# Kernel tuning notes

Hardware: AMD Instinct MI355X
Metric: run time of the kernel (lower is better)

Reference implementation:

```python
import jax, jax.numpy as jnp
import numpy as np

H_SP, W_SP = 8, 8
NUM_HEADS = 6
SHARED = 96
DIM_Q, DIM_KV = 96, 192
WIN = H_SP * W_SP  # 64 tokens per window


def _rel_index():
    # Swin-style relative position index, static numpy computation
    coords = np.stack(np.meshgrid(np.arange(H_SP), np.arange(W_SP), indexing='ij'))
    cf = coords.reshape(2, -1)                      # [2, 64]
    rel = cf[:, :, None] - cf[:, None, :]           # [2, 64, 64]
    rel = rel.transpose(1, 2, 0).astype(np.int64)   # [64, 64, 2]
    rel[..., 0] += H_SP - 1
    rel[..., 1] += W_SP - 1
    rel[..., 0] *= 2 * W_SP - 1
    return rel.sum(-1)                              # [64, 64], values in [0, 225)

REL_IDX = jnp.asarray(_rel_index())


def setup_inputs() -> dict:
    key = jax.random.key(0)
    ks = jax.random.split(key, 12)
    B, H, W = 4, 256, 256
    f32 = jnp.float32
    std = 0.02
    return {
        'x_q':  jax.random.normal(ks[0], (B, DIM_Q, H, W), f32),
        'x_kv': jax.random.normal(ks[1], (B, DIM_KV, H, W), f32),
        'Wq': jax.random.normal(ks[2], (DIM_Q, SHARED), f32) * std,
        'bq': jnp.zeros((SHARED,), f32),
        'Wk': jax.random.normal(ks[3], (DIM_KV, SHARED), f32) * std,
        'bk': jnp.zeros((SHARED,), f32),
        'Wv': jax.random.normal(ks[4], (DIM_KV, SHARED), f32) * std,
        'bv': jnp.zeros((SHARED,), f32),
        'bias_table': jax.random.normal(ks[5], ((2 * H_SP - 1) * (2 * W_SP - 1), NUM_HEADS), f32) * std,
        'Wo': jax.random.normal(ks[6], (SHARED, DIM_Q), f32) * std,
        'bo': jnp.zeros((DIM_Q,), f32),
    }


def reference(x_q, x_kv, Wq, bq, Wk, bk, Wv, bv, bias_table, Wo, bo):
    B, Cq, H, W = x_q.shape
    nH, nW = H // H_SP, W // W_SP  # H, W divisible by window -> pad is a no-op
    hd = SHARED // NUM_HEADS
    scale = hd ** -0.5

    def to_windows(img):
        C = img.shape[1]
        x = img.reshape(B, C, nH, H_SP, nW, W_SP)
        return x.transpose(0, 2, 4, 3, 5, 1).reshape(-1, WIN, C)

    qw = to_windows(x_q)    # [nWin, 64, Cq]
    kvw = to_windows(x_kv)  # [nWin, 64, Ckv]

    def heads(x):
        return x.reshape(-1, WIN, NUM_HEADS, hd).transpose(0, 2, 1, 3)  # [nWin, h, 64, hd]

    q = heads(qw @ Wq + bq)
    k = heads(kvw @ Wk + bk)
    v = heads(kvw @ Wv + bv)

    attn = jnp.einsum('whqd,whkd->whqk', q, k) * scale  # [nWin, h, 64, 64]
    rel_bias = bias_table[REL_IDX].transpose(2, 0, 1)   # [h, 64, 64]
    attn = jax.nn.softmax(attn + rel_bias[None], axis=-1)

    out = jnp.einsum('whqk,whkd->whqd', attn, v)        # [nWin, h, 64, hd]
    out = out.transpose(0, 2, 1, 3).reshape(-1, WIN, SHARED)
    out = out @ Wo + bo                                 # [nWin, 64, Cq]

    # windows2img
    out = out.reshape(B, nH, nW, H_SP, W_SP, Cq)
    out = out.transpose(0, 1, 3, 2, 4, 5).reshape(B, H, W, Cq)
    return out.transpose(0, 3, 1, 2)  # [B, Cq, H, W]
```

## Files before the change

kernel.cpp:

```cpp
#include <hip/hip_runtime.h>

typedef short short8 __attribute__((ext_vector_type(8)));
typedef float f32x4 __attribute__((ext_vector_type(4)));
typedef unsigned short ushort;

#define MFMA(a, b, c) __builtin_amdgcn_mfma_f32_16x16x32_bf16(a, b, c, 0, 0, 0)

#define WS_WQT 0
#define WS_WKT 9216
#define WS_WVT 27648
#define WS_WOT 46080
#define WS_BIAS 55296
#define WS_TOTAL 56646

#define STR_A 104
#define OFF_A 0
#define OFF_K16 13312
#define OFF_VT 25600
#define STR_VT 72
#define OFF_PQ 39424
#define P_STRIDE 72
#define OFF_BIAS 50688
#define LDS_BYTES 53392

__device__ __forceinline__ ushort f2bf(float x) {
    unsigned u = __float_as_uint(x);
    u = (u + 0x7FFFu + ((u >> 16) & 1u)) >> 16;
    return (ushort)u;
}
__device__ __forceinline__ float bf2f(ushort u) {
    return __uint_as_float(((unsigned)u) << 16);
}

__global__ void prep_weights(const float* __restrict__ Wq, const float* __restrict__ Wk,
                             const float* __restrict__ Wv, const float* __restrict__ Wo,
                             const float* __restrict__ btab, ushort* __restrict__ ws) {
    int idx = blockIdx.x * 256 + threadIdx.x;
    if (idx < WS_WKT) {
        int f = idx >> 9, w = idx & 511, lane = w >> 3, j = w & 7;
        int nt = f / 3, kt = f % 3;
        int n = nt * 16 + (lane & 15), k = kt * 32 + (lane >> 4) * 8 + j;
        ws[idx] = f2bf(Wq[k * 96 + n]);
    } else if (idx < WS_WVT) {
        int t = idx - WS_WKT;
        int f = t >> 9, w = t & 511, lane = w >> 3, j = w & 7;
        int kt6 = f / 6, nt = f % 6;
        int n = nt * 16 + (lane & 15), k = kt6 * 32 + (lane >> 4) * 8 + j;
        ws[idx] = f2bf(Wk[k * 96 + n]);
    } else if (idx < WS_WOT) {
        int t = idx - WS_WVT;
        int f = t >> 9, w = t & 511, lane = w >> 3, j = w & 7;
        int kt6 = f / 6, nt = f % 6;
        int n = nt * 16 + (lane & 15), k = kt6 * 32 + (lane >> 4) * 8 + j;
        ws[idx] = f2bf(Wv[k * 96 + n]);
    } else if (idx < WS_BIAS) {
        int t = idx - WS_WOT;
        int f = t >> 9, w = t & 511, lane = w >> 3, j = w & 7;
        int nt = f / 3, kt = f % 3;
        int n = nt * 16 + (lane & 15), k = kt * 32 + (lane >> 4) * 8 + j;
        ws[idx] = f2bf(Wo[k * 96 + n]);
    } else if (idx < WS_TOTAL) {
        ws[idx] = f2bf(btab[idx - WS_BIAS]);
    }
}

__global__ __launch_bounds__(256, 3) void swin_attn(
    const float* __restrict__ xq, const float* __restrict__ xkv,
    const float* __restrict__ bq, const float* __restrict__ bk,
    const float* __restrict__ bv, const float* __restrict__ bo,
    const ushort* __restrict__ ws, float* __restrict__ out)
{
    __shared__ __align__(16) char smem[LDS_BYTES];
    const int tid = threadIdx.x;
    const int wave = tid >> 6, lane = tid & 63;
    const int l15 = lane & 15, quad = lane >> 4;
    int wid = ((blockIdx.x & 7) << 9) | (blockIdx.x >> 3);
    const int b = wid >> 10;
    const int wh = (wid >> 5) & 31, ww = wid & 31;
    const int h0 = wh * 8, w0 = ww * 8;
    const int mt = wave;

    ushort* A     = (ushort*)(smem + OFF_A);
    ushort* k16   = (ushort*)(smem + OFF_K16);
    ushort* vt    = (ushort*)(smem + OFF_VT);
    ushort* ps    = (ushort*)(smem + OFF_PQ) + wave * (16 * P_STRIDE);
    ushort* qsc   = (ushort*)(smem + OFF_PQ + 9216) + wave * 256;
    ushort* biasl = (ushort*)(smem + OFF_BIAS);

    float bqr[6], bkr[6], bvr[6], bor[6];
    #pragma unroll
    for (int h = 0; h < 6; ++h) {
        bqr[h] = bq[h * 16 + l15]; bkr[h] = bk[h * 16 + l15];
        bvr[h] = bv[h * 16 + l15]; bor[h] = bo[h * 16 + l15];
    }

    int pc[3], pi[3];
    #pragma unroll
    for (int t = 0; t < 3; ++t) { int p = tid + t * 256; pc[t] = p % 96; pi[t] = p / 96; }

    const float* xkvb = xkv + (size_t)b * 192 * 65536;
    float4 pf[3][2];
    #pragma unroll
    for (int t = 0; t < 3; ++t) {
        const float* g = xkvb + (size_t)pc[t] * 65536 + (h0 + pi[t]) * 256 + w0;
        pf[t][0] = *(const float4*)g; pf[t][1] = *(const float4*)(g + 4);
    }
    for (int i = tid; i < 1350; i += 256) biasl[i] = ws[WS_BIAS + i];

    #pragma unroll
    for (int t = 0; t < 3; ++t) {
        int base = (pi[t] * 8) * STR_A + pc[t];
        A[base]             = f2bf(pf[t][0].x); A[base + STR_A]     = f2bf(pf[t][0].y);
        A[base + 2 * STR_A] = f2bf(pf[t][0].z); A[base + 3 * STR_A] = f2bf(pf[t][0].w);
        A[base + 4 * STR_A] = f2bf(pf[t][1].x); A[base + 5 * STR_A] = f2bf(pf[t][1].y);
        A[base + 6 * STR_A] = f2bf(pf[t][1].z); A[base + 7 * STR_A] = f2bf(pf[t][1].w);
    }
    __syncthreads();

    float4 pg[3][2];
    #pragma unroll
    for (int t = 0; t < 3; ++t) {
        const float* g = xkvb + (size_t)(96 + pc[t]) * 65536 + (h0 + pi[t]) * 256 + w0;
        pg[t][0] = *(const float4*)g; pg[t][1] = *(const float4*)(g + 4);
    }

    f32x4 accK[6], accV[6];
    #pragma unroll
    for (int n = 0; n < 6; ++n) { accK[n] = {}; accV[n] = {}; }
    const int arow = (mt * 16 + l15) * STR_A + quad * 8;
    #pragma unroll
    for (int kt = 0; kt < 3; ++kt) {
        short8 a = *(const short8*)(A + arow + kt * 32);
        #pragma unroll
        for (int nt = 0; nt < 6; ++nt) {
            short8 bk8 = *(const short8*)(ws + WS_WKT + (((kt * 6) + nt) * 64 + lane) * 8);
            accK[nt] = MFMA(a, bk8, accK[nt]);
            short8 bv8 = *(const short8*)(ws + WS_WVT + (((kt * 6) + nt) * 64 + lane) * 8);
            accV[nt] = MFMA(a, bv8, accV[nt]);
        }
    }
    __syncthreads();

    #pragma unroll
    for (int t = 0; t < 3; ++t) {
        int base = (pi[t] * 8) * STR_A + pc[t];
        A[base]             = f2bf(pg[t][0].x); A[base + STR_A]     = f2bf(pg[t][0].y);
        A[base + 2 * STR_A] = f2bf(pg[t][0].z); A[base + 3 * STR_A] = f2bf(pg[t][0].w);
        A[base + 4 * STR_A] = f2bf(pg[t][1].x); A[base + 5 * STR_A] = f2bf(pg[t][1].y);
        A[base + 6 * STR_A] = f2bf(pg[t][1].z); A[base + 7 * STR_A] = f2bf(pg[t][1].w);
    }
    __syncthreads();

    const float* xqb = xq + (size_t)b * 96 * 65536;
    #pragma unroll
    for (int t = 0; t < 3; ++t) {
        const float* g = xqb + (size_t)pc[t] * 65536 + (h0 + pi[t]) * 256 + w0;
        pf[t][0] = *(const float4*)g; pf[t][1] = *(const float4*)(g + 4);
    }

    #pragma unroll
    for (int kt = 0; kt < 3; ++kt) {
        short8 a = *(const short8*)(A + arow + kt * 32);
        #pragma unroll
        for (int nt = 0; nt < 6; ++nt) {
            short8 bk8 = *(const short8*)(ws + WS_WKT + ((((3 + kt) * 6) + nt) * 64 + lane) * 8);
            accK[nt] = MFMA(a, bk8, accK[nt]);
            short8 bv8 = *(const short8*)(ws + WS_WVT + ((((3 + kt) * 6) + nt) * 64 + lane) * 8);
            accV[nt] = MFMA(a, bv8, accV[nt]);
        }
    }
    #pragma unroll
    for (int nt = 0; nt < 6; ++nt) {
        ushort* dk = k16 + nt * (64 * 16) + (mt * 16 + quad * 4) * 16 + l15;
        ushort* dv = vt + nt * (16 * STR_VT) + l15 * STR_VT + (mt * 16 + quad * 4);
        #pragma unroll
        for (int r = 0; r < 4; ++r) {
            dk[r * 16] = f2bf(accK[nt][r] + bkr[nt]);
            dv[r]      = f2bf(accV[nt][r] + bvr[nt]);
        }
    }
    __syncthreads();

    #pragma unroll
    for (int t = 0; t < 3; ++t) {
        int base = (pi[t] * 8) * STR_A + pc[t];
        A[base]             = f2bf(pf[t][0].x); A[base + STR_A]     = f2bf(pf[t][0].y);
        A[base + 2 * STR_A] = f2bf(pf[t][0].z); A[base + 3 * STR_A] = f2bf(pf[t][0].w);
        A[base + 4 * STR_A] = f2bf(pf[t][1].x); A[base + 5 * STR_A] = f2bf(pf[t][1].y);
        A[base + 6 * STR_A] = f2bf(pf[t][1].z); A[base + 7 * STR_A] = f2bf(pf[t][1].w);
    }
    __syncthreads();

    const int qtok0 = mt * 16 + quad * 4;
    int bidx[4][4];
    #pragma unroll
    for (int nt = 0; nt < 4; ++nt) {
        int kt2 = nt * 16 + l15, i2 = kt2 >> 3, j2 = kt2 & 7;
        #pragma unroll
        for (int r = 0; r < 4; ++r) {
            int qt = qtok0 + r, i1 = qt >> 3, j1 = qt & 7;
            bidx[nt][r] = ((i1 - i2 + 7) * 15 + (j1 - j2 + 7)) * 6;
        }
    }

    f32x4 accO[6];
    short8 zero8 = {};
    for (int h = 0; h < 6; ++h) {
        f32x4 qa = {};
        #pragma unroll
        for (int kt = 0; kt < 3; ++kt) {
            short8 a  = *(const short8*)(A + arow + kt * 32);
            short8 bb = *(const short8*)(ws + WS_WQT + ((h * 3 + kt) * 64 + lane) * 8);
            qa = MFMA(a, bb, qa);
        }
        #pragma unroll
        for (int r = 0; r < 4; ++r)
            qsc[(quad * 4 + r) * 16 + l15] = f2bf((qa[r] + bqr[h]) * 0.25f);

        short8 aq = zero8;
        if (quad < 2) aq = *(const short8*)(qsc + l15 * 16 + quad * 8);
        f32x4 s[4];
        #pragma unroll
        for (int nt = 0; nt < 4; ++nt) {
            short8 bk8 = zero8;
            if (quad < 2) bk8 = *(const short8*)(k16 + h * (64 * 16) + (nt * 16 + l15) * 16 + quad * 8);
            f32x4 z = {};
            s[nt] = MFMA(aq, bk8, z);
        }
        #pragma unroll
        for (int nt = 0; nt < 4; ++nt)
            #pragma unroll
            for (int r = 0; r < 4; ++r)
                s[nt][r] += bf2f(biasl[bidx[nt][r] + h]);
        float pr[4][4];
        #pragma unroll
        for (int r = 0; r < 4; ++r) {
            float m = fmaxf(fmaxf(s[0][r], s[1][r]), fmaxf(s[2][r], s[3][r]));
            m = fmaxf(m, __shfl_xor(m, 1)); m = fmaxf(m, __shfl_xor(m, 2));
            m = fmaxf(m, __shfl_xor(m, 4)); m = fmaxf(m, __shfl_xor(m, 8));
            float l = 0.f;
            #pragma unroll
            for (int nt = 0; nt < 4; ++nt) { pr[nt][r] = __expf(s[nt][r] - m); l += pr[nt][r]; }
            l += __shfl_xor(l, 1); l += __shfl_xor(l, 2);
            l += __shfl_xor(l, 4); l += __shfl_xor(l, 8);
            float inv = 1.0f / l;
            #pragma unroll
            for (int nt = 0; nt < 4; ++nt) pr[nt][r] *= inv;
        }
        #pragma unroll
        for (int nt = 0; nt < 4; ++nt)
            #pragma unroll
            for (int r = 0; r < 4; ++r)
                ps[(quad * 4 + r) * P_STRIDE + nt * 16 + l15] = f2bf(pr[nt][r]);
        f32x4 o = {};
        #pragma unroll
        for (int k2 = 0; k2 < 2; ++k2) {
            short8 ap  = *(const short8*)(ps + l15 * P_STRIDE + k2 * 32 + quad * 8);
            short8 bv8 = *(const short8*)(vt + h * (16 * STR_VT) + l15 * STR_VT + k2 * 32 + quad * 8);
            o = MFMA(ap, bv8, o);
        }
        accO[h] = o;
    }
    __syncthreads();

    ushort* obuf = A;
    #pragma unroll
    for (int h = 0; h < 6; ++h)
        #pragma unroll
        for (int r = 0; r < 4; ++r)
            obuf[(mt * 16 + quad * 4 + r) * STR_A + h * 16 + l15] = f2bf(accO[h][r]);

    {
        int t0 = mt * 16 + quad * 4;
        int i = t0 >> 3, j0 = t0 & 7;
        #pragma unroll
        for (int nt = 0; nt < 6; ++nt) {
            f32x4 acc = {};
            #pragma unroll
            for (int kt = 0; kt < 3; ++kt) {
                short8 a  = *(const short8*)(obuf + arow + kt * 32);
                short8 bb = *(const short8*)(ws + WS_WOT + ((nt * 3 + kt) * 64 + lane) * 8);
                acc = MFMA(a, bb, acc);
            }
            int cout = nt * 16 + l15;
            float4 v4 = make_float4(acc[0] + bor[nt], acc[1] + bor[nt], acc[2] + bor[nt], acc[3] + bor[nt]);
            float* dst = out + (size_t)(b * 96 + cout) * 65536 + (h0 + i) * 256 + w0 + j0;
            *(float4*)dst = v4;
        }
    }
}

extern "C" void kernel_launch(void* const* d_in, const int* in_sizes, int n_in,
                              void* d_out, int out_size, void* d_ws, size_t ws_size,
                              hipStream_t stream) {
    const float* xq   = (const float*)d_in[0];
    const float* xkv  = (const float*)d_in[1];
    const float* Wq   = (const float*)d_in[2];
    const float* bq   = (const float*)d_in[3];
    const float* Wk   = (const float*)d_in[4];
    const float* bk   = (const float*)d_in[5];
    const float* Wv   = (const float*)d_in[6];
    const float* bv   = (const float*)d_in[7];
    const float* btab = (const float*)d_in[8];
    const float* Wo   = (const float*)d_in[9];
    const float* bo   = (const float*)d_in[10];
    ushort* ws = (ushort*)d_ws;
    float* out = (float*)d_out;

    hipLaunchKernelGGL(prep_weights, dim3((WS_TOTAL + 255) / 256), dim3(256), 0, stream,
                       Wq, Wk, Wv, Wo, btab, ws);
    hipLaunchKernelGGL(swin_attn, dim3(4096), dim3(256), 0, stream,
                       xq, xkv, bq, bk, bv, bo, ws, out);
}
```

Measured before the change: 513.6 us.

## Split fused window attention into projection, attention and output-projection kernels

```diff
diff --git a/kernel.cpp b/kernel.cpp
--- a/kernel.cpp
+++ b/kernel.cpp
@@ -6,65 +6,326 @@
 
 #define MFMA(a, b, c) __builtin_amdgcn_mfma_f32_16x16x32_bf16(a, b, c, 0, 0, 0)
 
-#define WS_WQT 0
-#define WS_WKT 9216
-#define WS_WVT 27648
-#define WS_WOT 46080
-#define WS_BIAS 55296
-#define WS_TOTAL 56646
-
+__device__ __forceinline__ ushort f2bf(float x) {
+    unsigned u = __float_as_uint(x);
+    u = (u + 0x7FFFu + ((u >> 16) & 1u)) >> 16;
+    return (ushort)u;
+}
+__device__ __forceinline__ float bf2f(ushort u) {
+    return __uint_as_float(((unsigned)u) << 16);
+}
+
+#define WS_Q   0
+#define WS_KV  9216
+#define WS_O   46080
+#define WS_BT  55296
+#define WS_BIG 56648
+#define QBUF_OFF  WS_BIG
+#define KVBUF_OFF (WS_BIG + 25165824)
+#define ABUF_OFF  (KVBUF_OFF + 50331648)
+#define NEED_BYTES ((size_t)(ABUF_OFF + 25165824) * 2)
+
+__global__ void prep_w(const float* __restrict__ Wq, const float* __restrict__ Wk,
+                       const float* __restrict__ Wv, const float* __restrict__ Wo,
+                       const float* __restrict__ btab, ushort* __restrict__ ws) {
+    int idx = blockIdx.x * 256 + threadIdx.x;
+    if (idx < WS_KV) {
+        int f = idx >> 9, w = idx & 511, lane = w >> 3, j = w & 7;
+        int kt = f / 6, nt = f % 6;
+        int cout = nt * 16 + (lane & 15), c = kt * 32 + (lane >> 4) * 8 + j;
+        ws[idx] = f2bf(Wq[c * 96 + cout] * 0.25f);
+    } else if (idx < WS_O) {
+        int t = idx - WS_KV; int f = t >> 9, w = t & 511, lane = w >> 3, j = w & 7;
+        int kt6 = f / 12, nt = f % 12;
+        int cout = nt * 16 + (lane & 15), c = kt6 * 32 + (lane >> 4) * 8 + j;
+        float v = (cout < 96) ? Wk[c * 96 + cout] : Wv[c * 96 + (cout - 96)];
+        ws[idx] = f2bf(v);
+    } else if (idx < WS_BT) {
+        int t = idx - WS_O; int f = t >> 9, w = t & 511, lane = w >> 3, j = w & 7;
+        int kt = f / 6, mt = f % 6;
+        int m = mt * 16 + (lane & 15), k = kt * 32 + (lane >> 4) * 8 + j;
+        ws[idx] = f2bf(Wo[k * 96 + m]);
+    } else if (idx < WS_BIG) {
+        if (idx < WS_BT + 1350) ws[idx] = f2bf(btab[idx - WS_BT]);
+    }
+}
+
+__global__ __launch_bounds__(256, 4) void k2_proj(
+    const float* __restrict__ xq, const float* __restrict__ xkv,
+    const float* __restrict__ bq, const float* __restrict__ bk,
+    const float* __restrict__ bv, const ushort* __restrict__ ws,
+    ushort* __restrict__ qbuf, ushort* __restrict__ kvbuf)
+{
+    __shared__ ushort At[64 * 104];
+    const int tid = threadIdx.x;
+    const int wave = tid >> 6, lane = tid & 63, l15 = lane & 15, quad = lane >> 4;
+    const bool isQ = blockIdx.x < 4096;
+    const int g = isQ ? blockIdx.x : blockIdx.x - 4096;
+    const int b = g >> 10, tok0 = (g & 1023) * 64;
+    const int arow = (wave * 16 + l15) * 104 + quad * 8;
+    const int trow = tok0 + wave * 16 + quad * 4;
+
+    if (isQ) {
+        const float* src = xq + (size_t)b * 96 * 65536;
+        #pragma unroll 4
+        for (int p = 0; p < 24; ++p) {
+            int c = p * 4 + wave;
+            At[lane * 104 + c] = f2bf(src[c * 65536 + tok0 + lane]);
+        }
+        __syncthreads();
+        f32x4 acc[6];
+        #pragma unroll
+        for (int n = 0; n < 6; ++n) acc[n] = {};
+        #pragma unroll
+        for (int kt = 0; kt < 3; ++kt) {
+            short8 a = *(const short8*)(At + arow + kt * 32);
+            #pragma unroll
+            for (int nt = 0; nt < 6; ++nt) {
+                short8 w8 = *(const short8*)(ws + WS_Q + ((kt * 6 + nt) * 64 + lane) * 8);
+                acc[nt] = MFMA(a, w8, acc[nt]);
+            }
+        }
+        ushort* dst = qbuf + ((size_t)b * 65536 + trow) * 96;
+        #pragma unroll
+        for (int nt = 0; nt < 6; ++nt) {
+            float bias = bq[nt * 16 + l15] * 0.25f;
+            #pragma unroll
+            for (int r = 0; r < 4; ++r)
+                dst[r * 96 + nt * 16 + l15] = f2bf(acc[nt][r] + bias);
+        }
+    } else {
+        const float* src = xkv + (size_t)b * 192 * 65536;
+        f32x4 acc[12];
+        #pragma unroll
+        for (int n = 0; n < 12; ++n) acc[n] = {};
+        for (int half = 0; half < 2; ++half) {
+            if (half) __syncthreads();
+            const float* s2 = src + half * 96 * 65536;
+            #pragma unroll 4
+            for (int p = 0; p < 24; ++p) {
+                int c = p * 4 + wave;
+                At[lane * 104 + c] = f2bf(s2[c * 65536 + tok0 + lane]);
+            }
+            __syncthreads();
+            #pragma unroll
+            for (int kt = 0; kt < 3; ++kt) {
+                short8 a = *(const short8*)(At + arow + kt * 32);
+                int kt6 = half * 3 + kt;
+                #pragma unroll
+                for (int nt = 0; nt < 12; ++nt) {
+                    short8 w8 = *(const short8*)(ws + WS_KV + ((kt6 * 12 + nt) * 64 + lane) * 8);
+                    acc[nt] = MFMA(a, w8, acc[nt]);
+                }
+            }
+        }
+        ushort* dst = kvbuf + ((size_t)b * 65536 + trow) * 192;
+        #pragma unroll
+        for (int nt = 0; nt < 12; ++nt) {
+            int cout = nt * 16 + l15;
+            float bias = (cout < 96) ? bk[cout] : bv[cout - 96];
+            #pragma unroll
+            for (int r = 0; r < 4; ++r)
+                dst[r * 192 + cout] = f2bf(acc[nt][r] + bias);
+        }
+    }
+}
+
+#define K3_VT 0
+#define K3_PS 13824
+#define K3_BIAS 26112
+#define K3_LDS 28812
+
+__global__ __launch_bounds__(256, 4) void k3_attn(
+    const ushort* __restrict__ ws, const ushort* __restrict__ qbuf,
+    const ushort* __restrict__ kvbuf, ushort* __restrict__ abuf)
+{
+    __shared__ __align__(16) char smem[K3_LDS];
+    ushort* vt    = (ushort*)smem;
+    ushort* biasl = (ushort*)(smem + K3_BIAS);
+    const int tid = threadIdx.x;
+    const int wave = tid >> 6, lane = tid & 63, l15 = lane & 15, quad = lane >> 4;
+    const int wid = blockIdx.x;
+    const int b = wid >> 10, wh = (wid >> 5) & 31, ww = wid & 31;
+    const int wb = b * 65536 + (wh * 8) * 256 + ww * 8;
+
+    for (int i = tid; i < 1350; i += 256) biasl[i] = ws[WS_BT + i];
+    {
+        int tok = tid >> 2, cc = tid & 3;
+        int tg = wb + (tok >> 3) * 256 + (tok & 7);
+        const ushort* vrow = kvbuf + (size_t)tg * 192 + 96;
+        #pragma unroll
+        for (int rd = 0; rd < 3; ++rd) {
+            int vd0 = (rd * 4 + cc) * 8;
+            short8 v8 = *(const short8*)(vrow + vd0);
+            #pragma unroll
+            for (int e = 0; e < 8; ++e)
+                vt[(vd0 + e) * 72 + tok] = (ushort)v8[e];
+        }
+    }
+    const int myq = wave * 16 + l15;
+    const size_t qrow = ((size_t)(wb + (myq >> 3) * 256 + (myq & 7))) * 96;
+    size_t krow[4];
+    #pragma unroll
+    for (int nt = 0; nt < 4; ++nt) {
+        int kt2 = nt * 16 + l15;
+        krow[nt] = ((size_t)(wb + (kt2 >> 3) * 256 + (kt2 & 7))) * 192;
+    }
+    const int qtok0 = wave * 16 + quad * 4;
+    int bidx[4][4];
+    #pragma unroll
+    for (int nt = 0; nt < 4; ++nt) {
+        int kt2 = nt * 16 + l15, i2 = kt2 >> 3, j2 = kt2 & 7;
+        #pragma unroll
+        for (int r = 0; r < 4; ++r) {
+            int qt = qtok0 + r, i1 = qt >> 3, j1 = qt & 7;
+            bidx[nt][r] = ((i1 - i2 + 7) * 15 + (j1 - j2 + 7)) * 6;
+        }
+    }
+    __syncthreads();
+
+    ushort* ps = (ushort*)(smem + K3_PS) + wave * 1152;
+    f32x4 accO[6];
+    short8 zero8 = {};
+    for (int h = 0; h < 6; ++h) {
+        short8 aq = zero8;
+        if (quad < 2) aq = *(const short8*)(qbuf + qrow + h * 16 + quad * 8);
+        f32x4 s[4];
+        #pragma unroll
+        for (int nt = 0; nt < 4; ++nt) {
+            short8 bk8 = zero8;
+            if (quad < 2) bk8 = *(const short8*)(kvbuf + krow[nt] + h * 16 + quad * 8);
+            f32x4 z = {};
+            s[nt] = MFMA(aq, bk8, z);
+        }
+        #pragma unroll
+        for (int nt = 0; nt < 4; ++nt)
+            #pragma unroll
+            for (int r = 0; r < 4; ++r)
+                s[nt][r] += bf2f(biasl[bidx[nt][r] + h]);
+        float pr[4][4];
+        #pragma unroll
+        for (int r = 0; r < 4; ++r) {
+            float m = fmaxf(fmaxf(s[0][r], s[1][r]), fmaxf(s[2][r], s[3][r]));
+            m = fmaxf(m, __shfl_xor(m, 1)); m = fmaxf(m, __shfl_xor(m, 2));
+            m = fmaxf(m, __shfl_xor(m, 4)); m = fmaxf(m, __shfl_xor(m, 8));
+            float l = 0.f;
+            #pragma unroll
+            for (int nt = 0; nt < 4; ++nt) { pr[nt][r] = __expf(s[nt][r] - m); l += pr[nt][r]; }
+            l += __shfl_xor(l, 1); l += __shfl_xor(l, 2);
+            l += __shfl_xor(l, 4); l += __shfl_xor(l, 8);
+            float inv = 1.0f / l;
+            #pragma unroll
+            for (int nt = 0; nt < 4; ++nt) pr[nt][r] *= inv;
+        }
+        #pragma unroll
+        for (int nt = 0; nt < 4; ++nt)
+            #pragma unroll
+            for (int r = 0; r < 4; ++r)
+                ps[(quad * 4 + r) * 72 + nt * 16 + l15] = f2bf(pr[nt][r]);
+        f32x4 o = {};
+        #pragma unroll
+        for (int k2 = 0; k2 < 2; ++k2) {
+            short8 ap  = *(const short8*)(ps + l15 * 72 + k2 * 32 + quad * 8);
+            short8 bv8 = *(const short8*)(vt + (h * 16 + l15) * 72 + k2 * 32 + quad * 8);
+            o = MFMA(ap, bv8, o);
+        }
+        accO[h] = o;
+    }
+    __syncthreads();
+
+    ushort* obuf = (ushort*)(smem + K3_PS);
+    #pragma unroll
+    for (int h = 0; h < 6; ++h)
+        #pragma unroll
+        for (int r = 0; r < 4; ++r)
+            obuf[(wave * 16 + quad * 4 + r) * 96 + h * 16 + l15] = f2bf(accO[h][r]);
+    #pragma unroll
+    for (int e = 0; e < 3; ++e) {
+        int cid = e * 64 + lane;
+        int tr = wave * 16 + cid / 12, c8 = cid % 12;
+        short8 o8 = *(const short8*)(obuf + tr * 96 + c8 * 8);
+        int tg = wb + (tr >> 3) * 256 + (tr & 7);
+        *(short8*)(abuf + (size_t)tg * 96 + c8 * 8) = o8;
+    }
+}
+
+__global__ __launch_bounds__(256, 4) void k4_out(
+    const ushort* __restrict__ ws, const ushort* __restrict__ abuf,
+    const float* __restrict__ bo, float* __restrict__ out)
+{
+    const int tid = threadIdx.x;
+    const int wave = tid >> 6, lane = tid & 63, l15 = lane & 15, quad = lane >> 4;
+    const int wtok = blockIdx.x * 64 + wave * 16;
+    const ushort* arow = abuf + (size_t)(wtok + l15) * 96;
+    f32x4 acc[6];
+    #pragma unroll
+    for (int m = 0; m < 6; ++m) acc[m] = {};
+    #pragma unroll
+    for (int kt = 0; kt < 3; ++kt) {
+        short8 bfrag = *(const short8*)(arow + kt * 32 + quad * 8);
+        #pragma unroll
+        for (int mt = 0; mt < 6; ++mt) {
+            short8 a8 = *(const short8*)(ws + WS_O + ((kt * 6 + mt) * 64 + lane) * 8);
+            acc[mt] = MFMA(a8, bfrag, acc[mt]);
+        }
+    }
+    const int b = wtok >> 16, rem = wtok & 65535;
+    #pragma unroll
+    for (int mt = 0; mt < 6; ++mt) {
+        float4 bo4 = *(const float4*)(bo + mt * 16 + quad * 4);
+        float bv[4] = {bo4.x, bo4.y, bo4.z, bo4.w};
+        #pragma unroll
+        for (int r = 0; r < 4; ++r) {
+            int cout = mt * 16 + quad * 4 + r;
+            out[(size_t)(b * 96 + cout) * 65536 + rem + l15] = acc[mt][r] + bv[r];
+        }
+    }
+}
+
+#define FB_WQT 0
+#define FB_WKT 9216
+#define FB_WVT 27648
+#define FB_WOT 46080
+#define FB_BIAS 55296
+#define FB_TOTAL 56646
 #define STR_A 104
 #define OFF_A 0
 #define OFF_K16 13312
 #define OFF_VT 25600
-#define STR_VT 72
 #define OFF_PQ 39424
-#define P_STRIDE 72
 #define OFF_BIAS 50688
 #define LDS_BYTES 53392
 
-__device__ __forceinline__ ushort f2bf(float x) {
-    unsigned u = __float_as_uint(x);
-    u = (u + 0x7FFFu + ((u >> 16) & 1u)) >> 16;
-    return (ushort)u;
-}
-__device__ __forceinline__ float bf2f(ushort u) {
-    return __uint_as_float(((unsigned)u) << 16);
-}
-
-__global__ void prep_weights(const float* __restrict__ Wq, const float* __restrict__ Wk,
-                             const float* __restrict__ Wv, const float* __restrict__ Wo,
-                             const float* __restrict__ btab, ushort* __restrict__ ws) {
+__global__ void prep_w_fb(const float* __restrict__ Wq, const float* __restrict__ Wk,
+                          const float* __restrict__ Wv, const float* __restrict__ Wo,
+                          const float* __restrict__ btab, ushort* __restrict__ ws) {
     int idx = blockIdx.x * 256 + threadIdx.x;
-    if (idx < WS_WKT) {
+    if (idx < FB_WKT) {
         int f = idx >> 9, w = idx & 511, lane = w >> 3, j = w & 7;
         int nt = f / 3, kt = f % 3;
         int n = nt * 16 + (lane & 15), k = kt * 32 + (lane >> 4) * 8 + j;
         ws[idx] = f2bf(Wq[k * 96 + n]);
-    } else if (idx < WS_WVT) {
-        int t = idx - WS_WKT;
-        int f = t >> 9, w = t & 511, lane = w >> 3, j = w & 7;
+    } else if (idx < FB_WVT) {
+        int t = idx - FB_WKT; int f = t >> 9, w = t & 511, lane = w >> 3, j = w & 7;
         int kt6 = f / 6, nt = f % 6;
         int n = nt * 16 + (lane & 15), k = kt6 * 32 + (lane >> 4) * 8 + j;
         ws[idx] = f2bf(Wk[k * 96 + n]);
-    } else if (idx < WS_WOT) {
-        int t = idx - WS_WVT;
-        int f = t >> 9, w = t & 511, lane = w >> 3, j = w & 7;
+    } else if (idx < FB_WOT) {
+        int t = idx - FB_WVT; int f = t >> 9, w = t & 511, lane = w >> 3, j = w & 7;
         int kt6 = f / 6, nt = f % 6;
         int n = nt * 16 + (lane & 15), k = kt6 * 32 + (lane >> 4) * 8 + j;
         ws[idx] = f2bf(Wv[k * 96 + n]);
-    } else if (idx < WS_BIAS) {
-        int t = idx - WS_WOT;
-        int f = t >> 9, w = t & 511, lane = w >> 3, j = w & 7;
+    } else if (idx < FB_BIAS) {
+        int t = idx - FB_WOT; int f = t >> 9, w = t & 511, lane = w >> 3, j = w & 7;
         int nt = f / 3, kt = f % 3;
         int n = nt * 16 + (lane & 15), k = kt * 32 + (lane >> 4) * 8 + j;
         ws[idx] = f2bf(Wo[k * 96 + n]);
-    } else if (idx < WS_TOTAL) {
-        ws[idx] = f2bf(btab[idx - WS_BIAS]);
-    }
-}
-
-__global__ __launch_bounds__(256, 3) void swin_attn(
+    } else if (idx < FB_TOTAL) {
+        ws[idx] = f2bf(btab[idx - FB_BIAS]);
+    }
+}
+
+__global__ __launch_bounds__(256, 3) void swin_attn_fb(
     const float* __restrict__ xq, const float* __restrict__ xkv,
     const float* __restrict__ bq, const float* __restrict__ bk,
     const float* __restrict__ bv, const float* __restrict__ bo,
@@ -79,25 +340,21 @@
     const int wh = (wid >> 5) & 31, ww = wid & 31;
     const int h0 = wh * 8, w0 = ww * 8;
     const int mt = wave;
-
     ushort* A     = (ushort*)(smem + OFF_A);
     ushort* k16   = (ushort*)(smem + OFF_K16);
     ushort* vt    = (ushort*)(smem + OFF_VT);
-    ushort* ps    = (ushort*)(smem + OFF_PQ) + wave * (16 * P_STRIDE);
+    ushort* ps    = (ushort*)(smem + OFF_PQ) + wave * (16 * 72);
     ushort* qsc   = (ushort*)(smem + OFF_PQ + 9216) + wave * 256;
     ushort* biasl = (ushort*)(smem + OFF_BIAS);
-
     float bqr[6], bkr[6], bvr[6], bor[6];
     #pragma unroll
     for (int h = 0; h < 6; ++h) {
         bqr[h] = bq[h * 16 + l15]; bkr[h] = bk[h * 16 + l15];
         bvr[h] = bv[h * 16 + l15]; bor[h] = bo[h * 16 + l15];
     }
-
     int pc[3], pi[3];
     #pragma unroll
     for (int t = 0; t < 3; ++t) { int p = tid + t * 256; pc[t] = p % 96; pi[t] = p / 96; }
-
     const float* xkvb = xkv + (size_t)b * 192 * 65536;
     float4 pf[3][2];
     #pragma unroll
@@ -105,25 +362,22 @@
         const float* g = xkvb + (size_t)pc[t] * 65536 + (h0 + pi[t]) * 256 + w0;
         pf[t][0] = *(const float4*)g; pf[t][1] = *(const float4*)(g + 4);
     }
-    for (int i = tid; i < 1350; i += 256) biasl[i] = ws[WS_BIAS + i];
-
+    for (int i = tid; i < 1350; i += 256) biasl[i] = ws[FB_BIAS + i];
     #pragma unroll
     for (int t = 0; t < 3; ++t) {
         int base = (pi[t] * 8) * STR_A + pc[t];
-        A[base]             = f2bf(pf[t][0].x); A[base + STR_A]     = f2bf(pf[t][0].y);
+        A[base] = f2bf(pf[t][0].x); A[base + STR_A] = f2bf(pf[t][0].y);
         A[base + 2 * STR_A] = f2bf(pf[t][0].z); A[base + 3 * STR_A] = f2bf(pf[t][0].w);
         A[base + 4 * STR_A] = f2bf(pf[t][1].x); A[base + 5 * STR_A] = f2bf(pf[t][1].y);
         A[base + 6 * STR_A] = f2bf(pf[t][1].z); A[base + 7 * STR_A] = f2bf(pf[t][1].w);
     }
     __syncthreads();
-
     float4 pg[3][2];
     #pragma unroll
     for (int t = 0; t < 3; ++t) {
         const float* g = xkvb + (size_t)(96 + pc[t]) * 65536 + (h0 + pi[t]) * 256 + w0;
         pg[t][0] = *(const float4*)g; pg[t][1] = *(const float4*)(g + 4);
     }
-
     f32x4 accK[6], accV[6];
     #pragma unroll
     for (int n = 0; n < 6; ++n) { accK[n] = {}; accV[n] = {}; }
@@ -133,46 +387,43 @@
         short8 a = *(const short8*)(A + arow + kt * 32);
         #pragma unroll
         for (int nt = 0; nt < 6; ++nt) {
-            short8 bk8 = *(const short8*)(ws + WS_WKT + (((kt * 6) + nt) * 64 + lane) * 8);
+            short8 bk8 = *(const short8*)(ws + FB_WKT + (((kt * 6) + nt) * 64 + lane) * 8);
             accK[nt] = MFMA(a, bk8, accK[nt]);
-            short8 bv8 = *(const short8*)(ws + WS_WVT + (((kt * 6) + nt) * 64 + lane) * 8);
+            short8 bv8 = *(const short8*)(ws + FB_WVT + (((kt * 6) + nt) * 64 + lane) * 8);
             accV[nt] = MFMA(a, bv8, accV[nt]);
         }
     }
     __syncthreads();
-
     #pragma unroll
     for (int t = 0; t < 3; ++t) {
         int base = (pi[t] * 8) * STR_A + pc[t];
-        A[base]             = f2bf(pg[t][0].x); A[base + STR_A]     = f2bf(pg[t][0].y);
+        A[base] = f2bf(pg[t][0].x); A[base + STR_A] = f2bf(pg[t][0].y);
         A[base + 2 * STR_A] = f2bf(pg[t][0].z); A[base + 3 * STR_A] = f2bf(pg[t][0].w);
         A[base + 4 * STR_A] = f2bf(pg[t][1].x); A[base + 5 * STR_A] = f2bf(pg[t][1].y);
         A[base + 6 * STR_A] = f2bf(pg[t][1].z); A[base + 7 * STR_A] = f2bf(pg[t][1].w);
     }
     __syncthreads();
-
     const float* xqb = xq + (size_t)b * 96 * 65536;
     #pragma unroll
     for (int t = 0; t < 3; ++t) {
         const float* g = xqb + (size_t)pc[t] * 65536 + (h0 + pi[t]) * 256 + w0;
         pf[t][0] = *(const float4*)g; pf[t][1] = *(const float4*)(g + 4);
     }
-
     #pragma unroll
     for (int kt = 0; kt < 3; ++kt) {
         short8 a = *(const short8*)(A + arow + kt * 32);
         #pragma unroll
         for (int nt = 0; nt < 6; ++nt) {
-            short8 bk8 = *(const short8*)(ws + WS_WKT + ((((3 + kt) * 6) + nt) * 64 + lane) * 8);
+            short8 bk8 = *(const short8*)(ws + FB_WKT + ((((3 + kt) * 6) + nt) * 64 + lane) * 8);
             accK[nt] = MFMA(a, bk8, accK[nt]);
-            short8 bv8 = *(const short8*)(ws + WS_WVT + ((((3 + kt) * 6) + nt) * 64 + lane) * 8);
+            short8 bv8 = *(const short8*)(ws + FB_WVT + ((((3 + kt) * 6) + nt) * 64 + lane) * 8);
             accV[nt] = MFMA(a, bv8, accV[nt]);
         }
     }
     #pragma unroll
     for (int nt = 0; nt < 6; ++nt) {
         ushort* dk = k16 + nt * (64 * 16) + (mt * 16 + quad * 4) * 16 + l15;
-        ushort* dv = vt + nt * (16 * STR_VT) + l15 * STR_VT + (mt * 16 + quad * 4);
+        ushort* dv = vt + nt * (16 * 72) + l15 * 72 + (mt * 16 + quad * 4);
         #pragma unroll
         for (int r = 0; r < 4; ++r) {
             dk[r * 16] = f2bf(accK[nt][r] + bkr[nt]);
@@ -180,17 +431,15 @@
         }
     }
     __syncthreads();
-
     #pragma unroll
     for (int t = 0; t < 3; ++t) {
         int base = (pi[t] * 8) * STR_A + pc[t];
-        A[base]             = f2bf(pf[t][0].x); A[base + STR_A]     = f2bf(pf[t][0].y);
+        A[base] = f2bf(pf[t][0].x); A[base + STR_A] = f2bf(pf[t][0].y);
         A[base + 2 * STR_A] = f2bf(pf[t][0].z); A[base + 3 * STR_A] = f2bf(pf[t][0].w);
         A[base + 4 * STR_A] = f2bf(pf[t][1].x); A[base + 5 * STR_A] = f2bf(pf[t][1].y);
         A[base + 6 * STR_A] = f2bf(pf[t][1].z); A[base + 7 * STR_A] = f2bf(pf[t][1].w);
     }
     __syncthreads();
-
     const int qtok0 = mt * 16 + quad * 4;
     int bidx[4][4];
     #pragma unroll
@@ -202,7 +451,6 @@
             bidx[nt][r] = ((i1 - i2 + 7) * 15 + (j1 - j2 + 7)) * 6;
         }
     }
-
     f32x4 accO[6];
     short8 zero8 = {};
     for (int h = 0; h < 6; ++h) {
@@ -210,13 +458,12 @@
         #pragma unroll
         for (int kt = 0; kt < 3; ++kt) {
             short8 a  = *(const short8*)(A + arow + kt * 32);
-            short8 bb = *(const short8*)(ws + WS_WQT + ((h * 3 + kt) * 64 + lane) * 8);
+            short8 bb = *(const short8*)(ws + FB_WQT + ((h * 3 + kt) * 64 + lane) * 8);
             qa = MFMA(a, bb, qa);
         }
         #pragma unroll
         for (int r = 0; r < 4; ++r)
             qsc[(quad * 4 + r) * 16 + l15] = f2bf((qa[r] + bqr[h]) * 0.25f);
-
         short8 aq = zero8;
         if (quad < 2) aq = *(const short8*)(qsc + l15 * 16 + quad * 8);
         f32x4 s[4];
@@ -251,25 +498,23 @@
         for (int nt = 0; nt < 4; ++nt)
             #pragma unroll
             for (int r = 0; r < 4; ++r)
-                ps[(quad * 4 + r) * P_STRIDE + nt * 16 + l15] = f2bf(pr[nt][r]);
+                ps[(quad * 4 + r) * 72 + nt * 16 + l15] = f2bf(pr[nt][r]);
         f32x4 o = {};
         #pragma unroll
         for (int k2 = 0; k2 < 2; ++k2) {
-            short8 ap  = *(const short8*)(ps + l15 * P_STRIDE + k2 * 32 + quad * 8);
-            short8 bv8 = *(const short8*)(vt + h * (16 * STR_VT) + l15 * STR_VT + k2 * 32 + quad * 8);
+            short8 ap  = *(const short8*)(ps + l15 * 72 + k2 * 32 + quad * 8);
+            short8 bv8 = *(const short8*)(vt + h * (16 * 72) + l15 * 72 + k2 * 32 + quad * 8);
             o = MFMA(ap, bv8, o);
         }
         accO[h] = o;
     }
     __syncthreads();
-
     ushort* obuf = A;
     #pragma unroll
     for (int h = 0; h < 6; ++h)
         #pragma unroll
         for (int r = 0; r < 4; ++r)
             obuf[(mt * 16 + quad * 4 + r) * STR_A + h * 16 + l15] = f2bf(accO[h][r]);
-
     {
         int t0 = mt * 16 + quad * 4;
         int i = t0 >> 3, j0 = t0 & 7;
@@ -279,7 +524,7 @@
             #pragma unroll
             for (int kt = 0; kt < 3; ++kt) {
                 short8 a  = *(const short8*)(obuf + arow + kt * 32);
-                short8 bb = *(const short8*)(ws + WS_WOT + ((nt * 3 + kt) * 64 + lane) * 8);
+                short8 bb = *(const short8*)(ws + FB_WOT + ((nt * 3 + kt) * 64 + lane) * 8);
                 acc = MFMA(a, bb, acc);
             }
             int cout = nt * 16 + l15;
@@ -307,8 +552,18 @@
     ushort* ws = (ushort*)d_ws;
     float* out = (float*)d_out;
 
-    hipLaunchKernelGGL(prep_weights, dim3((WS_TOTAL + 255) / 256), dim3(256), 0, stream,
-                       Wq, Wk, Wv, Wo, btab, ws);
-    hipLaunchKernelGGL(swin_attn, dim3(4096), dim3(256), 0, stream,
-                       xq, xkv, bq, bk, bv, bo, ws, out);
-}
+    if (ws_size >= NEED_BYTES) {
+        ushort* qbuf  = ws + QBUF_OFF;
+        ushort* kvbuf = ws + KVBUF_OFF;
+        ushort* abuf  = ws + ABUF_OFF;
+        hipLaunchKernelGGL(prep_w, dim3(222), dim3(256), 0, stream, Wq, Wk, Wv, Wo, btab, ws);
+        hipLaunchKernelGGL(k2_proj, dim3(8192), dim3(256), 0, stream,
+                           xq, xkv, bq, bk, bv, ws, qbuf, kvbuf);
+        hipLaunchKernelGGL(k3_attn, dim3(4096), dim3(256), 0, stream, ws, qbuf, kvbuf, abuf);
+        hipLaunchKernelGGL(k4_out, dim3(4096), dim3(256), 0, stream, ws, abuf, bo, out);
+    } else {
+        hipLaunchKernelGGL(prep_w_fb, dim3(222), dim3(256), 0, stream, Wq, Wk, Wv, Wo, btab, ws);
+        hipLaunchKernelGGL(swin_attn_fb, dim3(4096), dim3(256), 0, stream,
+                           xq, xkv, bq, bk, bv, bo, ws, out);
+    }
+}
```

Result: slower. 561.5 us (+9.3%).
